# Kernel optimization log

Hardware: AMD Instinct MI355X
Metric: run time of the kernel (lower is better)

The kernel has to match this reference:

```python
import jax, jax.numpy as jnp
import numpy as np

K = 5  # filter_size (matches init_kwargs)


def _adaptive_pool_matrix(size: int, k: int) -> jnp.ndarray:
    """Row-stochastic [k, size] matrix replicating torch adaptive_avg_pool1d bins."""
    P = np.zeros((k, size), np.float32)
    for i in range(k):
        s = (i * size) // k
        e = -((-(i + 1) * size) // k)  # ceil((i+1)*size/k)
        P[i, s:e] = 1.0 / (e - s)
    return jnp.asarray(P)


def setup_inputs() -> dict:
    key = jax.random.key(0)
    k1, k2, k3 = jax.random.split(key, 3)
    B, Cin, Cout, H, W = 8, 32, 32, 256, 256
    x = jax.random.normal(k1, (B, Cin, H, W), jnp.float32)
    conv_w = jax.random.normal(k2, (Cout, Cin), jnp.float32) * (1.0 / np.sqrt(Cin))
    conv_b = jax.random.normal(k3, (Cout,), jnp.float32) * 0.01
    return {"x": x, "conv_w": conv_w, "conv_b": conv_b}


def reference(x, conv_w, conv_b):
    B, Cin, H, W = x.shape
    # 1x1 conv == channel-mixing einsum
    feat = jnp.einsum('bihw,oi->bohw', x, conv_w) + conv_b[None, :, None, None]
    C = feat.shape[1]
    # adaptive_avg_pool2d(feat, K) via static pooling matrices -> per-(b,c) KxK filter
    Ph = _adaptive_pool_matrix(H, K)
    Pw = _adaptive_pool_matrix(W, K)
    filt = jnp.einsum('kh,bchw,lw->bckl', Ph, feat, Pw)  # [B, C, K, K]
    # pad per original intent ('same' output), then grouped conv with groups=B*C
    pad = (K - 1) // 2
    if (K - 1) % 2 == 0:
        p = ((pad, pad), (pad, pad))
    else:
        p = ((pad + 1, pad), (pad + 1, pad))
    inp = feat.reshape(1, B * C, H, W)
    w = filt.reshape(B * C, 1, K, K)
    out = jax.lax.conv_general_dilated(
        inp, w, window_strides=(1, 1), padding=p,
        dimension_numbers=('NCHW', 'OIHW', 'NCHW'),
        feature_group_count=B * C)
    return out.reshape(B, C, H, W)
```

## Files before the change

kernel.cpp:

```cpp
#include <hip/hip_runtime.h>


#define CIN 32
#define COUT 32
#define HW 256
#define PLANE (HW * HW)
#define BATCH 8
#define KF 5
#define BIN 52

__global__ __launch_bounds__(256) void conv1x1_pool_kernel(const float* __restrict__ x,
                                                           const float* __restrict__ Wm,
                                                           const float* __restrict__ bias,
                                                           float* __restrict__ feat,
                                                           float* __restrict__ filt_raw) {
    int b   = blockIdx.x >> 8;
    int row = blockIdx.x & 255;
    int t   = threadIdx.x;

    __shared__ __align__(16) float lds[CIN * HW];

    const float* xb = x + (size_t)b * CIN * PLANE + row * HW;
#pragma unroll
    for (int j = 0; j < 8; ++j) {
        int idx = t + 256 * j;
        int ch  = idx >> 6;
        int c4  = (idx & 63) << 2;
        *(float4*)&lds[ch * HW + c4] = *(const float4*)(xb + (size_t)ch * PLANE + c4);
    }
    __syncthreads();

    float acc[COUT];
#pragma unroll
    for (int o = 0; o < COUT; ++o) acc[o] = bias[o];
#pragma unroll
    for (int i = 0; i < CIN; ++i) {
        float xi = lds[i * HW + t];
#pragma unroll
        for (int o = 0; o < COUT; ++o) acc[o] += Wm[o * CIN + i] * xi;
    }

    float* fb = feat + (size_t)b * COUT * PLANE + row * HW + t;
#pragma unroll
    for (int o = 0; o < COUT; ++o) fb[(size_t)o * PLANE] = acc[o];

    __syncthreads();
#pragma unroll
    for (int o = 0; o < COUT; ++o) lds[o * HW + t] = acc[o];
    __syncthreads();

    if (t < COUT * KF) {
        int o  = t / KF;
        int l  = t - o * KF;
        int sl = (l * HW) / KF;
        float s = 0.f;
        for (int w = 0; w < BIN; ++w) s += lds[o * HW + sl + w];
        float* dst = filt_raw + (size_t)(b * COUT + o) * 25 + l;
#pragma unroll
        for (int k = 0; k < KF; ++k) {
            int sk = (k * HW) / KF;
            if (row >= sk && row < sk + BIN) atomicAdd(dst + k * KF, s);
        }
    }
}

#define LROW 264
__global__ __launch_bounds__(256) void dwconv_kernel(const float* __restrict__ feat,
                                                     const float* __restrict__ filt_raw,
                                                     float* __restrict__ out) {
    int bo    = blockIdx.y;
    int strip = blockIdx.x;
    int gy0   = strip * 32;
    int t     = threadIdx.x;

    __shared__ __align__(16) float s[36 * LROW];
    __shared__ float sfilt[25];
    if (t < 25) sfilt[t] = filt_raw[bo * 25 + t] * (1.0f / (52.0f * 52.0f));
    if (t < 144) {
        int lr = t >> 2, e = t & 3;
        int ci = (e < 2) ? (2 + e) : (258 + e);
        s[lr * LROW + ci] = 0.f;
    }

    const float* fb = feat + (size_t)bo * PLANE;
#pragma unroll
    for (int j = 0; j < 9; ++j) {
        int idx = t + 256 * j;
        int lr  = idx >> 6;
        int cx  = (idx & 63) * 4;
        int gy  = gy0 - 2 + lr;
        float4 v = {0.f, 0.f, 0.f, 0.f};
        if ((unsigned)gy < (unsigned)HW) v = *(const float4*)(fb + gy * HW + cx);
        *(float4*)(&s[lr * LROW + 4 + cx]) = v;
    }
    __syncthreads();

    float fw[25];
#pragma unroll
    for (int j = 0; j < 25; ++j) fw[j] = sfilt[j];

    int c = t;
    float w0[5], w1[5], w2[5], w3[5], w4[5];
#pragma unroll
    for (int j = 0; j < 5; ++j) {
        w0[j] = s[0 * LROW + 2 + c + j];
        w1[j] = s[1 * LROW + 2 + c + j];
        w2[j] = s[2 * LROW + 2 + c + j];
        w3[j] = s[3 * LROW + 2 + c + j];
    }
    float* ob = out + (size_t)bo * PLANE + (size_t)gy0 * HW + c;
#pragma unroll
    for (int r = 0; r < 32; ++r) {
#pragma unroll
        for (int j = 0; j < 5; ++j) w4[j] = s[(r + 4) * LROW + 2 + c + j];
        float acc = 0.f;
#pragma unroll
        for (int j = 0; j < 5; ++j) {
            acc += fw[0 * 5 + j] * w0[j];
            acc += fw[1 * 5 + j] * w1[j];
            acc += fw[2 * 5 + j] * w2[j];
            acc += fw[3 * 5 + j] * w3[j];
            acc += fw[4 * 5 + j] * w4[j];
        }
        ob[r * HW] = acc;
#pragma unroll
        for (int j = 0; j < 5; ++j) {
            w0[j] = w1[j]; w1[j] = w2[j]; w2[j] = w3[j]; w3[j] = w4[j];
        }
    }
}

extern "C" void kernel_launch(void* const* d_in, const int* in_sizes, int n_in,
                              void* d_out, int out_size, void* d_ws, size_t ws_size,
                              hipStream_t stream) {
    const float* x      = (const float*)d_in[0];
    const float* conv_w = (const float*)d_in[1];
    const float* conv_b = (const float*)d_in[2];
    float* out = (float*)d_out;

    float* feat = (float*)d_ws;
    float* filt = feat + (size_t)BATCH * COUT * PLANE;

    hipMemsetAsync(filt, 0, BATCH * COUT * 25 * sizeof(float), stream);
    conv1x1_pool_kernel<<<dim3(BATCH * 256), dim3(256), 0, stream>>>(x, conv_w, conv_b, feat, filt);
    dwconv_kernel<<<dim3(8, BATCH * COUT), dim3(256), 0, stream>>>(feat, filt, out);
}
```

Baseline: 156.9 us.

## Pool input x before conv and derive filters via linearity

Uses the linearity of the 1x1 conv to pool the input x directly into per-channel 5x5 bins in a separate kernel, then builds the filters inside the depthwise kernel as W*xpool + bias. This replaces the heavy per-row atomic pooling of conv outputs. The conv kernel also drops its LDS staging and has each thread compute two pixels with float2 loads. The cost is reading x an extra time in a new kernel launch.

```diff
diff --git a/kernel.cpp b/kernel.cpp
--- a/kernel.cpp
+++ b/kernel.cpp
@@ -9,73 +9,101 @@
 #define KF 5
 #define BIN 52
 
-__global__ __launch_bounds__(256) void conv1x1_pool_kernel(const float* __restrict__ x,
-                                                           const float* __restrict__ Wm,
-                                                           const float* __restrict__ bias,
-                                                           float* __restrict__ feat,
-                                                           float* __restrict__ filt_raw) {
-    int b   = blockIdx.x >> 8;
-    int row = blockIdx.x & 255;
-    int t   = threadIdx.x;
+__global__ __launch_bounds__(256) void pool_x_kernel(const float* __restrict__ x,
+                                                     float* __restrict__ xpool) {
+    int blk   = blockIdx.x;
+    int s     = blk & 7;
+    int plane = blk >> 3;
+    int t     = threadIdx.x;
+    int gy0   = s * 32;
 
-    __shared__ __align__(16) float lds[CIN * HW];
+    const float* xp = x + (size_t)plane * PLANE + (size_t)gy0 * HW + t;
+    float acc[KF] = {0.f, 0.f, 0.f, 0.f, 0.f};
+#pragma unroll
+    for (int r = 0; r < 32; ++r) {
+        float v  = xp[(size_t)r * HW];
+        int   gy = gy0 + r;
+#pragma unroll
+        for (int k = 0; k < KF; ++k) {
+            const int sk = (k * HW) / KF;
+            if (gy >= sk && gy < sk + BIN) acc[k] += v;
+        }
+    }
 
-    const float* xb = x + (size_t)b * CIN * PLANE + row * HW;
+    __shared__ float lds[KF][HW + 1];
 #pragma unroll
-    for (int j = 0; j < 8; ++j) {
-        int idx = t + 256 * j;
-        int ch  = idx >> 6;
-        int c4  = (idx & 63) << 2;
-        *(float4*)&lds[ch * HW + c4] = *(const float4*)(xb + (size_t)ch * PLANE + c4);
-    }
+    for (int k = 0; k < KF; ++k) lds[k][t] = acc[k];
     __syncthreads();
 
-    float acc[COUT];
+    if (t < KF * KF) {
+        int kk = t / KF, ll = t - kk * KF;
+        int sl = (ll * HW) / KF;
+        float ssum = 0.f;
+#pragma unroll 4
+        for (int w = 0; w < BIN; ++w) ssum += lds[kk][sl + w];
+        atomicAdd(&xpool[plane * 25 + t], ssum);
+    }
+}
+
+__global__ __launch_bounds__(256) void conv_kernel(const float* __restrict__ x,
+                                                   const float* __restrict__ Wm,
+                                                   const float* __restrict__ bias,
+                                                   float* __restrict__ feat) {
+    int blk = blockIdx.x;
+    int b   = blk >> 7;
+    int rp  = blk & 127;
+    int t   = threadIdx.x;
+    int row = rp * 2 + (t >> 7);
+    int c2  = (t & 127) * 2;
+
+    const float* xb = x + (size_t)b * CIN * PLANE + (size_t)row * HW + c2;
+
+    float a0[COUT], a1[COUT];
 #pragma unroll
-    for (int o = 0; o < COUT; ++o) acc[o] = bias[o];
+    for (int o = 0; o < COUT; ++o) { float bv = bias[o]; a0[o] = bv; a1[o] = bv; }
+
 #pragma unroll
     for (int i = 0; i < CIN; ++i) {
-        float xi = lds[i * HW + t];
+        float2 xv = *(const float2*)(xb + (size_t)i * PLANE);
 #pragma unroll
-        for (int o = 0; o < COUT; ++o) acc[o] += Wm[o * CIN + i] * xi;
+        for (int o = 0; o < COUT; ++o) {
+            float w = Wm[o * CIN + i];
+            a0[o] += w * xv.x;
+            a1[o] += w * xv.y;
+        }
     }
 
-    float* fb = feat + (size_t)b * COUT * PLANE + row * HW + t;
+    float* fb = feat + (size_t)b * COUT * PLANE + (size_t)row * HW + c2;
 #pragma unroll
-    for (int o = 0; o < COUT; ++o) fb[(size_t)o * PLANE] = acc[o];
-
-    __syncthreads();
-#pragma unroll
-    for (int o = 0; o < COUT; ++o) lds[o * HW + t] = acc[o];
-    __syncthreads();
-
-    if (t < COUT * KF) {
-        int o  = t / KF;
-        int l  = t - o * KF;
-        int sl = (l * HW) / KF;
-        float s = 0.f;
-        for (int w = 0; w < BIN; ++w) s += lds[o * HW + sl + w];
-        float* dst = filt_raw + (size_t)(b * COUT + o) * 25 + l;
-#pragma unroll
-        for (int k = 0; k < KF; ++k) {
-            int sk = (k * HW) / KF;
-            if (row >= sk && row < sk + BIN) atomicAdd(dst + k * KF, s);
-        }
+    for (int o = 0; o < COUT; ++o) {
+        float2 v; v.x = a0[o]; v.y = a1[o];
+        *(float2*)(fb + (size_t)o * PLANE) = v;
     }
 }
 
 #define LROW 264
 __global__ __launch_bounds__(256) void dwconv_kernel(const float* __restrict__ feat,
-                                                     const float* __restrict__ filt_raw,
+                                                     const float* __restrict__ xpool,
+                                                     const float* __restrict__ Wm,
+                                                     const float* __restrict__ bias,
                                                      float* __restrict__ out) {
     int bo    = blockIdx.y;
+    int b     = bo >> 5;
+    int o     = bo & 31;
     int strip = blockIdx.x;
     int gy0   = strip * 32;
     int t     = threadIdx.x;
 
     __shared__ __align__(16) float s[36 * LROW];
     __shared__ float sfilt[25];
-    if (t < 25) sfilt[t] = filt_raw[bo * 25 + t] * (1.0f / (52.0f * 52.0f));
+
+    if (t < 25) {
+        float acc = bias[o] * 2704.0f;
+        const float* xp = xpool + (size_t)b * CIN * 25 + t;
+#pragma unroll
+        for (int i = 0; i < CIN; ++i) acc += Wm[o * CIN + i] * xp[i * 25];
+        sfilt[t] = acc * (1.0f / 2704.0f);
+    }
     if (t < 144) {
         int lr = t >> 2, e = t & 3;
         int ci = (e < 2) ? (2 + e) : (258 + e);
@@ -90,7 +118,7 @@
         int cx  = (idx & 63) * 4;
         int gy  = gy0 - 2 + lr;
         float4 v = {0.f, 0.f, 0.f, 0.f};
-        if ((unsigned)gy < (unsigned)HW) v = *(const float4*)(fb + gy * HW + cx);
+        if ((unsigned)gy < (unsigned)HW) v = *(const float4*)(fb + (size_t)gy * HW + cx);
         *(float4*)(&s[lr * LROW + 4 + cx]) = v;
     }
     __syncthreads();
@@ -122,7 +150,7 @@
             acc += fw[3 * 5 + j] * w3[j];
             acc += fw[4 * 5 + j] * w4[j];
         }
-        ob[r * HW] = acc;
+        ob[(size_t)r * HW] = acc;
 #pragma unroll
         for (int j = 0; j < 5; ++j) {
             w0[j] = w1[j]; w1[j] = w2[j]; w2[j] = w3[j]; w3[j] = w4[j];
@@ -138,10 +166,11 @@
     const float* conv_b = (const float*)d_in[2];
     float* out = (float*)d_out;
 
-    float* feat = (float*)d_ws;
-    float* filt = feat + (size_t)BATCH * COUT * PLANE;
+    float* feat  = (float*)d_ws;
+    float* xpool = feat + (size_t)BATCH * COUT * PLANE;
 
-    hipMemsetAsync(filt, 0, BATCH * COUT * 25 * sizeof(float), stream);
-    conv1x1_pool_kernel<<<dim3(BATCH * 256), dim3(256), 0, stream>>>(x, conv_w, conv_b, feat, filt);
-    dwconv_kernel<<<dim3(8, BATCH * COUT), dim3(256), 0, stream>>>(feat, filt, out);
+    hipMemsetAsync(xpool, 0, BATCH * CIN * 25 * sizeof(float), stream);
+    pool_x_kernel<<<dim3(2048), dim3(256), 0, stream>>>(x, xpool);
+    conv_kernel<<<dim3(1024), dim3(256), 0, stream>>>(x, conv_w, conv_b, feat);
+    dwconv_kernel<<<dim3(8, BATCH * COUT), dim3(256), 0, stream>>>(feat, xpool, conv_w, conv_b, out);
 }
```

Result: slower. 189.7 us (+20.9%).
